# Performance work log

Hardware: AMD Instinct MI355X
Metric: run time of the kernel (lower is better)

## Reference

```python
import jax, jax.numpy as jnp
import numpy as np

B, C, HH, WW = 16, 256, 64, 64
K, H, U, R = 16, 4, 4, 23
DIM_OUT = 256
DV = DIM_OUT // H  # 64
N = HH * WW
EPS = 1e-3  # keras BatchNormalization default epsilon


def setup_inputs() -> dict:
    key = jax.random.key(0)
    ks = jax.random.split(key, 16)
    sc = 0.02
    return {
        "x": jax.random.normal(ks[0], (B, C, HH, WW), jnp.float32),
        "w_q": jax.random.normal(ks[1], (K * H, C), jnp.float32) * sc,
        "w_k": jax.random.normal(ks[2], (K * U, C), jnp.float32) * sc,
        "w_v": jax.random.normal(ks[3], (DV * U, C), jnp.float32) * sc,
        "gamma_q": jnp.ones((K * H,), jnp.float32),
        "beta_q": jnp.zeros((K * H,), jnp.float32),
        "mean_q": jax.random.normal(ks[4], (K * H,), jnp.float32) * 0.1,
        "var_q": jax.random.uniform(ks[5], (K * H,), jnp.float32) + 0.5,
        "gamma_v": jnp.ones((DV * U,), jnp.float32),
        "beta_v": jnp.zeros((DV * U,), jnp.float32),
        "mean_v": jax.random.normal(ks[6], (DV * U,), jnp.float32) * 0.1,
        "var_v": jax.random.uniform(ks[7], (DV * U,), jnp.float32) + 0.5,
        "w_pos": jax.random.normal(ks[8], (K, U, 1, R, R), jnp.float32) * sc,
        "b_pos": jnp.zeros((K,), jnp.float32),
    }


def _bn(x, gamma, beta, mean, var):
    # inference-mode batchnorm over channel axis 1, x: [b,c,h,w]
    inv = gamma * jax.lax.rsqrt(var + EPS)
    return x * inv[None, :, None, None] + (beta - mean * inv)[None, :, None, None]


def reference(x, w_q, w_k, w_v, gamma_q, beta_q, mean_q, var_q,
              gamma_v, beta_v, mean_v, var_v, w_pos, b_pos):
    b = x.shape[0]
    # 1x1 conv projections (channels-first)
    q = jnp.einsum('oc,bchw->bohw', w_q, x)
    k = jnp.einsum('oc,bchw->bohw', w_k, x)
    v = jnp.einsum('oc,bchw->bohw', w_v, x)
    q = _bn(q, gamma_q, beta_q, mean_q, var_q)
    v = _bn(v, gamma_v, beta_v, mean_v, var_v)
    # rearrange to sequence form
    q = q.reshape(b, H, K, N)           # b h k n
    k = k.reshape(b, U, K, N)           # b u k m
    v = v.reshape(b, U, DV, N)          # b u v m
    k = jax.nn.softmax(k, axis=-1)      # softmax over positions m
    # content lambda
    Lc = jnp.einsum('bukm,buvm->bkv', k, v)
    Yc = jnp.einsum('bhkn,bkv->bnhv', q, Lc)
    # position lambda via local 3D conv over (v, hh, ww) with kernel (1, r, r)
    v5 = v.reshape(b, U, DV, HH, WW)
    Lp = jax.lax.conv_general_dilated(
        v5, w_pos, window_strides=(1, 1, 1),
        padding=[(0, 0), (R // 2, R // 2), (R // 2, R // 2)],
        dimension_numbers=('NCDHW', 'OIDHW', 'NCDHW'))
    Lp = Lp + b_pos[None, :, None, None, None]
    Lp = Lp.reshape(b, K, DV, N)        # b k v n
    Yp = jnp.einsum('bhkn,bkvn->bnhv', q, Lp)
    Y = Yc + Yp                          # [b, n, h, v]
    out = Y.transpose(0, 2, 3, 1).reshape(b, H * DV, HH, WW)
    return out
```

## Files before the change

### kernel.cpp

```cpp
#include <hip/hip_runtime.h>
#include <stdint.h>

#define EPS 1e-3f

typedef _Float16 f16x8 __attribute__((ext_vector_type(8)));
typedef float f32x4 __attribute__((ext_vector_type(4)));
typedef float f32x16 __attribute__((ext_vector_type(16)));

__global__ __launch_bounds__(256) void setup_kernel(
    const float* __restrict__ w_pos,
    const float* __restrict__ w_q, const float* __restrict__ w_k,
    const float* __restrict__ w_v,
    const float* __restrict__ gq, const float* __restrict__ bq,
    const float* __restrict__ mq, const float* __restrict__ vq,
    const float* __restrict__ gv, const float* __restrict__ bv,
    const float* __restrict__ mv, const float* __restrict__ vvar,
    float* __restrict__ scale_bias, float* __restrict__ Lc,
    _Float16* __restrict__ Wp, _Float16* __restrict__ Apack) {
  const int idx = blockIdx.x * 256 + threadIdx.x;
  if (idx < 384) {
    float sc, bi;
    if (idx < 64) {
      const float inv = gq[idx] * rsqrtf(vq[idx] + EPS);
      sc = inv; bi = bq[idx] - mq[idx] * inv;
    } else if (idx < 128) {
      sc = 1.f; bi = 0.f;
    } else {
      const int o = idx - 128;
      const float inv = gv[o] * rsqrtf(vvar[o] + EPS);
      sc = inv; bi = bv[o] - mv[o] * inv;
    }
    scale_bias[idx] = sc;
    scale_bias[384 + idx] = bi;
  }
  if (idx < 16384) Lc[idx] = 0.f;
  if (idx < 98304) {
    const int j = idx & 7;
    const int lane = (idx >> 3) & 63;
    const int fr = idx >> 9;
    const int kt = fr & 15;
    const int mt = fr >> 4;
    const int m = mt * 32 + (lane & 31);
    const int k = kt * 16 + (lane >> 5) * 8 + j;
    float sc; const float* Wsrc;
    if (m < 64) {
      sc = gq[m] * rsqrtf(vq[m] + EPS);
      Wsrc = w_q + (size_t)m * 256;
    } else if (m < 128) {
      sc = 1.f;
      Wsrc = w_k + (size_t)(m - 64) * 256;
    } else {
      const int r = m - 128;
      sc = gv[r] * rsqrtf(vvar[r] + EPS);
      Wsrc = w_v + (size_t)r * 256;
    }
    Wp[idx] = (_Float16)(Wsrc[k] * sc);
  }
  if (idx < 376832) {
    const int j = idx & 7;
    const int lane = (idx >> 3) & 63;
    const int f = idx >> 9;
    const int rel = f & 7;
    const int ss = (f >> 3) % 23;
    const int w = (f >> 3) / 23;
    const int m = lane & 31;
    const int kk = m & 15;
    const int ol = m >> 4;
    const int kap = lane >> 5;
    const int k = kap * 8 + j;
    const int u = k >> 2;
    const int y4 = k & 3;
    const int dy = 4 * rel + y4 - 2 * w - ol;
    float val = 0.f;
    if (dy >= 0 && dy < 23)
      val = w_pos[kk * 2116 + u * 529 + dy * 23 + ss];
    Apack[idx] = (_Float16)val;
  }
}

__global__ __launch_bounds__(256) void proj_gemm(
    const float* __restrict__ x, const _Float16* __restrict__ Wp,
    const float* __restrict__ scale_bias, float* __restrict__ projq,
    _Float16* __restrict__ projkv) {
  const int b = blockIdx.y;
  const int n0 = blockIdx.x * 32;
  const int tid = threadIdx.x;
  const int w = tid >> 6, lane = tid & 63;
  const int col = lane & 31, kap = lane >> 5;

  __shared__ __align__(16) _Float16 xT[32][264];

#pragma unroll
  for (int r = 0; r < 8; ++r) {
    const int i = tid + r * 256;
    const int k = i >> 3, n4 = (i & 7) * 4;
    const float4 xv = *(const float4*)&x[((size_t)(b * 256 + k)) * 4096 + n0 + n4];
    xT[n4 + 0][k] = (_Float16)xv.x;
    xT[n4 + 1][k] = (_Float16)xv.y;
    xT[n4 + 2][k] = (_Float16)xv.z;
    xT[n4 + 3][k] = (_Float16)xv.w;
  }
  __syncthreads();

  f32x16 acc[3];
#pragma unroll
  for (int i = 0; i < 3; ++i) acc[i] = (f32x16)0.f;

  const f16x8* Wf = (const f16x8*)Wp;
#pragma unroll
  for (int kt = 0; kt < 16; ++kt) {
    const f16x8 B =
        *(const f16x8*)__builtin_assume_aligned(&xT[col][kt * 16 + kap * 8], 16);
#pragma unroll
    for (int i = 0; i < 3; ++i) {
      const f16x8 A = Wf[(size_t)(((w * 3 + i) * 16 + kt) * 64) + lane];
      acc[i] = __builtin_amdgcn_mfma_f32_32x32x16_f16(A, B, acc[i], 0, 0, 0);
    }
  }

#pragma unroll
  for (int i = 0; i < 3; ++i) {
    const int mt = w * 3 + i;
#pragma unroll
    for (int reg = 0; reg < 16; ++reg) {
      const int row = (reg & 3) + 8 * (reg >> 2) + 4 * kap;
      const int o = mt * 32 + row;
      const float val = acc[i][reg] + scale_bias[384 + o];
      if (mt < 2)
        projq[((size_t)(b * 64 + o)) * 4096 + n0 + col] = val;
      else
        projkv[((size_t)(b * 320 + (o - 64))) * 4096 + n0 + col] = (_Float16)val;
    }
  }
}

__global__ __launch_bounds__(256) void kstats_kernel(
    const _Float16* __restrict__ projkv, float* __restrict__ kstat) {
  const int row = blockIdx.x;
  const int b = row >> 6, c = row & 63;
  const f16x8* p8 = (const f16x8*)(projkv + ((size_t)(b * 320 + c)) * 4096);
  const int tid = threadIdx.x;

  f16x8 h[2];
  h[0] = p8[tid];
  h[1] = p8[tid + 256];
  float vmax = -3.4e38f;
#pragma unroll
  for (int i = 0; i < 2; ++i)
#pragma unroll
    for (int e = 0; e < 8; ++e) vmax = fmaxf(vmax, (float)h[i][e]);
#pragma unroll
  for (int off = 32; off > 0; off >>= 1) vmax = fmaxf(vmax, __shfl_xor(vmax, off));
  __shared__ float redm[4], reds[4];
  if ((tid & 63) == 0) redm[tid >> 6] = vmax;
  __syncthreads();
  vmax = fmaxf(fmaxf(redm[0], redm[1]), fmaxf(redm[2], redm[3]));

  float sum = 0.f;
#pragma unroll
  for (int i = 0; i < 2; ++i)
#pragma unroll
    for (int e = 0; e < 8; ++e) sum += expf((float)h[i][e] - vmax);
#pragma unroll
  for (int off = 32; off > 0; off >>= 1) sum += __shfl_xor(sum, off);
  if ((tid & 63) == 0) reds[tid >> 6] = sum;
  __syncthreads();
  sum = reds[0] + reds[1] + reds[2] + reds[3];
  if (tid == 0) {
    kstat[(size_t)row * 2 + 0] = vmax;
    kstat[(size_t)row * 2 + 1] = 1.f / sum;
  }
}

__global__ __launch_bounds__(256) void lc_kernel(
    const _Float16* __restrict__ projkv, const float* __restrict__ kstat,
    float* __restrict__ Lc) {
  const int mc = blockIdx.x, b = blockIdx.y;
  const int m0 = mc * 128;
  const int tid = threadIdx.x;
  const int kk = tid & 15;
  const int dvb = tid >> 4;

  __shared__ float kT[16][132];
  __shared__ float vT[64][132];

  float a0 = 0.f, a1 = 0.f, a2 = 0.f, a3 = 0.f;

  for (int u = 0; u < 4; ++u) {
    __syncthreads();
    {
      const int row = tid >> 4, c8 = (tid & 15) * 8;
      const int ch = u * 16 + row;
      const float kmax = kstat[((size_t)b * 64 + ch) * 2 + 0];
      const float kinv = kstat[((size_t)b * 64 + ch) * 2 + 1];
      const f16x8 raw =
          *(const f16x8*)&projkv[((size_t)(b * 320 + ch)) * 4096 + m0 + c8];
#pragma unroll
      for (int e = 0; e < 8; ++e)
        kT[row][c8 + e] = expf((float)raw[e] - kmax) * kinv;
    }
#pragma unroll
    for (int r = 0; r < 4; ++r) {
      const int i = tid + r * 256;
      const int row = i >> 4, c8 = (i & 15) * 8;
      const f16x8 raw =
          *(const f16x8*)&projkv[((size_t)(b * 320 + 64 + u * 64 + row)) * 4096 + m0 + c8];
#pragma unroll
      for (int e = 0; e < 8; ++e) vT[row][c8 + e] = (float)raw[e];
    }
    __syncthreads();
#pragma unroll 4
    for (int m = 0; m < 128; ++m) {
      const float kv = kT[kk][m];
      a0 = fmaf(kv, vT[dvb * 4 + 0][m], a0);
      a1 = fmaf(kv, vT[dvb * 4 + 1][m], a1);
      a2 = fmaf(kv, vT[dvb * 4 + 2][m], a2);
      a3 = fmaf(kv, vT[dvb * 4 + 3][m], a3);
    }
  }

  float* dst = &Lc[((size_t)(b * 16 + kk)) * 64 + dvb * 4];
  atomicAdd(dst + 0, a0);
  atomicAdd(dst + 1, a1);
  atomicAdd(dst + 2, a2);
  atomicAdd(dst + 3, a3);
}

template <int W>
__device__ __forceinline__ void conv_worker(
    const _Float16* __restrict__ vL, const f16x8* __restrict__ Awl,
    const float* __restrict__ qsec, const float* __restrict__ lcb,
    const int n, const int kap, const int b, const int dv,
    float* __restrict__ out) {
  constexpr bool G0 = (W < 2);
  constexpr bool G6 = (W != 0);
  constexpr bool G7 = (W == 3);

  f16x8 A[8];
  if (G0) A[0] = Awl[0 * 64];
#pragma unroll
  for (int r = 1; r < 6; ++r) A[r] = Awl[r * 64];
  if (G6) A[6] = Awl[6 * 64];
  if (G7) A[7] = Awl[7 * 64];

#pragma unroll 1
  for (int pass = 0; pass < 2; ++pass) {
    f32x16 acc[8];
#pragma unroll
    for (int t = 0; t < 8; t++) acc[t] = (f32x16)0.f;

#pragma unroll 1
    for (int ss = 0; ss < 23; ++ss) {
      const int ssn = (ss == 22) ? 0 : ss + 1;
      const f16x8* Awn = Awl + (size_t)(ssn * 8) * 64;
      const _Float16* brow = &vL[(32 * pass + n + ss) * 360 + 8 * kap];

      f16x8 Bq[22];
      if (G0) Bq[0] = *(const f16x8*)__builtin_assume_aligned(brow, 16);
#pragma unroll
      for (int tau = 1; tau < 4; ++tau)
        Bq[tau] = *(const f16x8*)__builtin_assume_aligned(brow + 16 * tau, 16);

#pragma unroll
      for (int tau = 0; tau < 22; ++tau) {
        const int tpf = tau + 4;
        if (tpf < 22) {
          const bool live = (tpf == 20) ? G6 : (tpf == 21) ? G7 : true;
          if (live)
            Bq[tpf] = *(const f16x8*)__builtin_assume_aligned(brow + 16 * tpf, 16);
        }
        __builtin_amdgcn_s_setprio(1);
#pragma unroll
        for (int t = 0; t < 8; ++t) {
          const int rel = tau - 2 * t;
          if (rel < 0 || rel > 7) continue;
          if ((rel == 0 && !G0) || (rel == 6 && !G6) || (rel == 7 && !G7)) continue;
          acc[t] = __builtin_amdgcn_mfma_f32_32x32x16_f16(A[rel], Bq[tau], acc[t], 0, 0, 0);
        }
        __builtin_amdgcn_s_setprio(0);
        if (tau >= 14) {
          const int rn = tau - 14;
          const bool live = (rn == 0) ? G0 : (rn == 6) ? G6 : (rn == 7) ? G7 : true;
          if (live) A[rn] = Awn[rn * 64];
        }
      }
    }

    const int c = 32 * pass + n;
#pragma unroll 1
    for (int t = 0; t < 8; ++t) {
#pragma unroll
      for (int ol = 0; ol < 2; ++ol) {
        const int gamma = 8 * t + 2 * W + ol;
        const float* qg = qsec + (size_t)gamma * 64 + c;
        float y0 = 0.f, y1 = 0.f, y2 = 0.f, y3 = 0.f;
#pragma unroll
        for (int e = 0; e < 8; ++e) {
          const int kk = (e & 3) + 8 * (e >> 2) + 4 * kap;
          const float cf = acc[t][ol * 8 + e] + lcb[e];
          y0 = fmaf(qg[(size_t)(kk) * 4096], cf, y0);
          y1 = fmaf(qg[(size_t)(16 + kk) * 4096], cf, y1);
          y2 = fmaf(qg[(size_t)(32 + kk) * 4096], cf, y2);
          y3 = fmaf(qg[(size_t)(48 + kk) * 4096], cf, y3);
        }
        y0 += __shfl_xor(y0, 32);
        y1 += __shfl_xor(y1, 32);
        y2 += __shfl_xor(y2, 32);
        y3 += __shfl_xor(y3, 32);
        const float s0 = kap ? y2 : y0;
        const float s1 = kap ? y3 : y1;
        out[((size_t)(b * 256 + (2 * kap + 0) * 64 + dv)) * 4096 + gamma * 64 + c] = s0;
        out[((size_t)(b * 256 + (2 * kap + 1) * 64 + dv)) * 4096 + gamma * 64 + c] = s1;
      }
    }
  }
}

__global__ __launch_bounds__(256, 2) void lambda_conv(
    const float* __restrict__ projq, const _Float16* __restrict__ projkv,
    const _Float16* __restrict__ Apack,
    const float* __restrict__ Lc, const float* __restrict__ b_pos,
    float* __restrict__ out) {
  const int dv = blockIdx.x;
  const int b = blockIdx.y;
  const int tid = threadIdx.x;
  const int w = tid >> 6;
  const int lane = tid & 63;
  const int n = lane & 31;
  const int kap = lane >> 5;

  __shared__ __align__(16) _Float16 vL[86 * 360];

  {
    const uint4 z = {0u, 0u, 0u, 0u};
    for (int i = tid; i < (86 * 360 * 2) / 16; i += 256) ((uint4*)vL)[i] = z;
  }
  __syncthreads();

  {
    const _Float16* vsec = projkv + ((size_t)(b * 320 + 64 + dv)) * 4096;
    for (int idx = tid; idx < 2048; idx += 256) {
      const int u = idx >> 9, g = (idx >> 3) & 63, c8 = (idx & 7) * 8;
      const f16x8 vv = *(const f16x8*)&vsec[(size_t)u * 262144 + g * 64 + c8];
      const int sy = g + 11;
      const int qoff = (sy >> 2) * 16 + (u << 2) + (sy & 3);
      _Float16* base = &vL[(c8 + 11) * 360 + qoff];
#pragma unroll
      for (int e = 0; e < 8; ++e) base[(size_t)e * 360] = vv[e];
    }
  }
  __syncthreads();

  float lcb[8];
#pragma unroll
  for (int e = 0; e < 8; e++) {
    const int kk = (e & 3) + 8 * (e >> 2) + 4 * kap;
    lcb[e] = Lc[(b * 16 + kk) * 64 + dv] + b_pos[kk];
  }

  const float* qsec = projq + ((size_t)(b * 64)) * 4096;
  const f16x8* Ap = (const f16x8*)Apack;
  const f16x8* Awl = Ap + (size_t)(w * 184) * 64 + lane;

  switch (w) {
    case 0: conv_worker<0>(vL, Awl, qsec, lcb, n, kap, b, dv, out); break;
    case 1: conv_worker<1>(vL, Awl, qsec, lcb, n, kap, b, dv, out); break;
    case 2: conv_worker<2>(vL, Awl, qsec, lcb, n, kap, b, dv, out); break;
    default: conv_worker<3>(vL, Awl, qsec, lcb, n, kap, b, dv, out); break;
  }
}

extern "C" void kernel_launch(void* const* d_in, const int* in_sizes, int n_in,
                              void* d_out, int out_size, void* d_ws, size_t ws_size,
                              hipStream_t stream) {
  const float* x       = (const float*)d_in[0];
  const float* w_q     = (const float*)d_in[1];
  const float* w_k     = (const float*)d_in[2];
  const float* w_v     = (const float*)d_in[3];
  const float* gamma_q = (const float*)d_in[4];
  const float* beta_q  = (const float*)d_in[5];
  const float* mean_q  = (const float*)d_in[6];
  const float* var_q   = (const float*)d_in[7];
  const float* gamma_v = (const float*)d_in[8];
  const float* beta_v  = (const float*)d_in[9];
  const float* mean_v  = (const float*)d_in[10];
  const float* var_v   = (const float*)d_in[11];
  const float* w_pos   = (const float*)d_in[12];
  const float* b_pos   = (const float*)d_in[13];

  float* ws = (float*)d_ws;
  float* projq = ws;
  _Float16* projkv = (_Float16*)(ws + 4194304);
  float* sb = ws + 4194304 + 10485760;
  float* Lc = sb + 768;
  _Float16* Apack = (_Float16*)(Lc + 16384);
  _Float16* Wp = Apack + 376832;
  float* kstat = (float*)(Wp + 98304);
  float* out = (float*)d_out;

  setup_kernel<<<1472, 256, 0, stream>>>(w_pos, w_q, w_k, w_v,
                                         gamma_q, beta_q, mean_q, var_q,
                                         gamma_v, beta_v, mean_v, var_v,
                                         sb, Lc, Wp, Apack);
  proj_gemm<<<dim3(128, 16), 256, 0, stream>>>(x, Wp, sb, projq, projkv);
  kstats_kernel<<<1024, 256, 0, stream>>>(projkv, kstat);
  lc_kernel<<<dim3(32, 16), 256, 0, stream>>>(projkv, kstat, Lc);
  lambda_conv<<<dim3(64, 16), 256, 0, stream>>>(projq, projkv, Apack, Lc, b_pos, out);
}
```

Baseline: 510.3 us.

## Fuse softmax key statistics into projection GEMM and widen its N tile

```diff
diff --git a/kernel.cpp b/kernel.cpp
--- a/kernel.cpp
+++ b/kernel.cpp
@@ -16,6 +16,7 @@
     const float* __restrict__ gv, const float* __restrict__ bv,
     const float* __restrict__ mv, const float* __restrict__ vvar,
     float* __restrict__ scale_bias, float* __restrict__ Lc,
+    float* __restrict__ kstat,
     _Float16* __restrict__ Wp, _Float16* __restrict__ Apack) {
   const int idx = blockIdx.x * 256 + threadIdx.x;
   if (idx < 384) {
@@ -34,6 +35,7 @@
     scale_bias[384 + idx] = bi;
   }
   if (idx < 16384) Lc[idx] = 0.f;
+  if (idx < 1024) kstat[idx] = 0.f;
   if (idx < 98304) {
     const int j = idx & 7;
     const int lane = (idx >> 3) & 63;
@@ -81,19 +83,19 @@
 __global__ __launch_bounds__(256) void proj_gemm(
     const float* __restrict__ x, const _Float16* __restrict__ Wp,
     const float* __restrict__ scale_bias, float* __restrict__ projq,
-    _Float16* __restrict__ projkv) {
+    _Float16* __restrict__ projkv, float* __restrict__ kstat) {
   const int b = blockIdx.y;
-  const int n0 = blockIdx.x * 32;
+  const int n0 = blockIdx.x * 64;
   const int tid = threadIdx.x;
   const int w = tid >> 6, lane = tid & 63;
   const int col = lane & 31, kap = lane >> 5;
 
-  __shared__ __align__(16) _Float16 xT[32][264];
-
-#pragma unroll
-  for (int r = 0; r < 8; ++r) {
+  __shared__ __align__(16) _Float16 xT[64][264];
+
+#pragma unroll
+  for (int r = 0; r < 16; ++r) {
     const int i = tid + r * 256;
-    const int k = i >> 3, n4 = (i & 7) * 4;
+    const int k = i >> 4, n4 = (i & 15) * 4;
     const float4 xv = *(const float4*)&x[((size_t)(b * 256 + k)) * 4096 + n0 + n4];
     xT[n4 + 0][k] = (_Float16)xv.x;
     xT[n4 + 1][k] = (_Float16)xv.y;
@@ -102,19 +104,25 @@
   }
   __syncthreads();
 
-  f32x16 acc[3];
-#pragma unroll
-  for (int i = 0; i < 3; ++i) acc[i] = (f32x16)0.f;
+  f32x16 acc[3][2];
+#pragma unroll
+  for (int i = 0; i < 3; ++i) {
+    acc[i][0] = (f32x16)0.f;
+    acc[i][1] = (f32x16)0.f;
+  }
 
   const f16x8* Wf = (const f16x8*)Wp;
 #pragma unroll
   for (int kt = 0; kt < 16; ++kt) {
-    const f16x8 B =
+    const f16x8 B0 =
         *(const f16x8*)__builtin_assume_aligned(&xT[col][kt * 16 + kap * 8], 16);
+    const f16x8 B1 =
+        *(const f16x8*)__builtin_assume_aligned(&xT[col + 32][kt * 16 + kap * 8], 16);
 #pragma unroll
     for (int i = 0; i < 3; ++i) {
       const f16x8 A = Wf[(size_t)(((w * 3 + i) * 16 + kt) * 64) + lane];
-      acc[i] = __builtin_amdgcn_mfma_f32_32x32x16_f16(A, B, acc[i], 0, 0, 0);
+      acc[i][0] = __builtin_amdgcn_mfma_f32_32x32x16_f16(A, B0, acc[i][0], 0, 0, 0);
+      acc[i][1] = __builtin_amdgcn_mfma_f32_32x32x16_f16(A, B1, acc[i][1], 0, 0, 0);
     }
   }
 
@@ -125,50 +133,23 @@
     for (int reg = 0; reg < 16; ++reg) {
       const int row = (reg & 3) + 8 * (reg >> 2) + 4 * kap;
       const int o = mt * 32 + row;
-      const float val = acc[i][reg] + scale_bias[384 + o];
-      if (mt < 2)
-        projq[((size_t)(b * 64 + o)) * 4096 + n0 + col] = val;
-      else
-        projkv[((size_t)(b * 320 + (o - 64))) * 4096 + n0 + col] = (_Float16)val;
-    }
-  }
-}
-
-__global__ __launch_bounds__(256) void kstats_kernel(
-    const _Float16* __restrict__ projkv, float* __restrict__ kstat) {
-  const int row = blockIdx.x;
-  const int b = row >> 6, c = row & 63;
-  const f16x8* p8 = (const f16x8*)(projkv + ((size_t)(b * 320 + c)) * 4096);
-  const int tid = threadIdx.x;
-
-  f16x8 h[2];
-  h[0] = p8[tid];
-  h[1] = p8[tid + 256];
-  float vmax = -3.4e38f;
-#pragma unroll
-  for (int i = 0; i < 2; ++i)
-#pragma unroll
-    for (int e = 0; e < 8; ++e) vmax = fmaxf(vmax, (float)h[i][e]);
-#pragma unroll
-  for (int off = 32; off > 0; off >>= 1) vmax = fmaxf(vmax, __shfl_xor(vmax, off));
-  __shared__ float redm[4], reds[4];
-  if ((tid & 63) == 0) redm[tid >> 6] = vmax;
-  __syncthreads();
-  vmax = fmaxf(fmaxf(redm[0], redm[1]), fmaxf(redm[2], redm[3]));
-
-  float sum = 0.f;
-#pragma unroll
-  for (int i = 0; i < 2; ++i)
-#pragma unroll
-    for (int e = 0; e < 8; ++e) sum += expf((float)h[i][e] - vmax);
-#pragma unroll
-  for (int off = 32; off > 0; off >>= 1) sum += __shfl_xor(sum, off);
-  if ((tid & 63) == 0) reds[tid >> 6] = sum;
-  __syncthreads();
-  sum = reds[0] + reds[1] + reds[2] + reds[3];
-  if (tid == 0) {
-    kstat[(size_t)row * 2 + 0] = vmax;
-    kstat[(size_t)row * 2 + 1] = 1.f / sum;
+      const float bi = scale_bias[384 + o];
+      const float v0 = acc[i][0][reg] + bi;
+      const float v1 = acc[i][1][reg] + bi;
+      if (mt < 2) {
+        projq[((size_t)(b * 64 + o)) * 4096 + n0 + col] = v0;
+        projq[((size_t)(b * 64 + o)) * 4096 + n0 + 32 + col] = v1;
+      } else {
+        projkv[((size_t)(b * 320 + (o - 64))) * 4096 + n0 + col] = (_Float16)v0;
+        projkv[((size_t)(b * 320 + (o - 64))) * 4096 + n0 + 32 + col] = (_Float16)v1;
+        if (mt < 4) {
+          float s = expf(v0) + expf(v1);
+#pragma unroll
+          for (int off = 16; off > 0; off >>= 1) s += __shfl_xor(s, off);
+          if (col == 0) atomicAdd(&kstat[b * 64 + (o - 64)], s);
+        }
+      }
+    }
   }
 }
 
@@ -191,13 +172,12 @@
     {
       const int row = tid >> 4, c8 = (tid & 15) * 8;
       const int ch = u * 16 + row;
-      const float kmax = kstat[((size_t)b * 64 + ch) * 2 + 0];
-      const float kinv = kstat[((size_t)b * 64 + ch) * 2 + 1];
+      const float kinv = 1.f / kstat[(size_t)b * 64 + ch];
       const f16x8 raw =
           *(const f16x8*)&projkv[((size_t)(b * 320 + ch)) * 4096 + m0 + c8];
 #pragma unroll
       for (int e = 0; e < 8; ++e)
-        kT[row][c8 + e] = expf((float)raw[e] - kmax) * kinv;
+        kT[row][c8 + e] = expf((float)raw[e]) * kinv;
     }
 #pragma unroll
     for (int r = 0; r < 4; ++r) {
@@ -401,9 +381,8 @@
   setup_kernel<<<1472, 256, 0, stream>>>(w_pos, w_q, w_k, w_v,
                                          gamma_q, beta_q, mean_q, var_q,
                                          gamma_v, beta_v, mean_v, var_v,
-                                         sb, Lc, Wp, Apack);
-  proj_gemm<<<dim3(128, 16), 256, 0, stream>>>(x, Wp, sb, projq, projkv);
-  kstats_kernel<<<1024, 256, 0, stream>>>(projkv, kstat);
+                                         sb, Lc, kstat, Wp, Apack);
+  proj_gemm<<<dim3(64, 16), 256, 0, stream>>>(x, Wp, sb, projq, projkv, kstat);
   lc_kernel<<<dim3(32, 16), 256, 0, stream>>>(projkv, kstat, Lc);
   lambda_conv<<<dim3(64, 16), 256, 0, stream>>>(projq, projkv, Apack, Lc, b_pos, out);
 }
```

Result: slower. 536.4 us (+5.1%).
